# Kernel optimization log

Measured on AMD Instinct MI355X. Metric: run time of the kernel, lower is better.

The kernel has to match this reference:

```python
import jax, jax.numpy as jnp
import numpy as np

N = 8192
IN_DIM = 256
HID = 512
NUM_CLASSES = 256
AVG_DEG = 32


def setup_inputs() -> dict:
    key = jax.random.key(0)
    k_a, k_x, k_w1, k_w2 = jax.random.split(key, 4)
    # Binary adjacency with avg degree ~AVG_DEG (entries are exactly 1.0, matching
    # A.nonzero() edge extraction with implicit unit edge weights).
    A = (jax.random.uniform(k_a, (N, N)) < (AVG_DEG / N)).astype(jnp.float32)
    x = jax.random.normal(k_x, (N, IN_DIM), dtype=jnp.float32)
    # GCNConv params: glorot-ish weights, zero bias.
    W1 = jax.random.normal(k_w1, (IN_DIM, HID), dtype=jnp.float32) / np.sqrt(IN_DIM)
    b1 = jnp.zeros((HID,), dtype=jnp.float32)
    W2 = jax.random.normal(k_w2, (HID, NUM_CLASSES), dtype=jnp.float32) / np.sqrt(HID)
    b2 = jnp.zeros((NUM_CLASSES,), dtype=jnp.float32)
    sigmoid_param = jnp.array([10.0], dtype=jnp.float32)
    return {"A": A, "x": x, "W1": W1, "b1": b1, "W2": W2, "b2": b2,
            "sigmoid_param": sigmoid_param}


def _gcn_propagate(A, deg_inv_sqrt, h):
    # PyG GCNConv aggregation with self-loops, without materializing A + I:
    # out_j = d_j^{-1/2} * sum_i A_ij d_i^{-1/2} h_i  +  d_j^{-1} h_j
    m = deg_inv_sqrt[:, None] * h              # [N, d]
    agg = A.T @ m                              # messages flow row -> col
    return deg_inv_sqrt[:, None] * agg + (deg_inv_sqrt[:, None] ** 2) * h


def reference(A, x, W1, b1, W2, b2, sigmoid_param):
    # Degree from column sums of (A + I) — matches gcn_norm's scatter on col.
    deg = jnp.sum(A, axis=0) + 1.0             # [N], >= 1 thanks to self-loop
    deg_inv_sqrt = jax.lax.rsqrt(deg)
    skip_x = x                                  # nn.Identity skip connection
    # GCNConv 1: linear then normalized aggregation, then bias; ReLU.
    h = _gcn_propagate(A, deg_inv_sqrt, x @ W1) + b1
    h = jax.nn.relu(h)
    # GCNConv 2.
    h = _gcn_propagate(A, deg_inv_sqrt, h @ W2) + b2
    # Skip add + scaled sigmoid (original casts to double; kept float32 here).
    return jax.nn.sigmoid(sigmoid_param * (h + skip_x))
```

## Files before the change

kernel.cpp:

```cpp
#include <hip/hip_runtime.h>
#include <hip/hip_bf16.h>

#define N_NODES 8192
#define IN_DIM  256
#define HID     512
#define NCLS    256
#define CAP     128
#define LDSK    (HID + 8)

typedef __attribute__((ext_vector_type(8))) __bf16 bf16x8;
typedef __attribute__((ext_vector_type(4))) float  floatx4;

static __device__ __forceinline__ float bf2f(ushort u) {
    union { float f; unsigned int i; } v; v.i = ((unsigned int)u) << 16; return v.f;
}
static __device__ __forceinline__ ushort f2bf(float f) {
    __hip_bfloat16 b = __float2bfloat16(f);
    return *reinterpret_cast<ushort*>(&b);
}
static __device__ __forceinline__ void bfpair(unsigned int u, float& lo, float& hi) {
    union { float f; unsigned int i; } a, b;
    a.i = u << 16; b.i = u & 0xFFFF0000u;
    lo = a.f; hi = b.f;
}

__global__ __launch_bounds__(256) void build_csc(const float* __restrict__ A,
                                                 int* __restrict__ col_cnt,
                                                 int* __restrict__ col_idx) {
    const int jbase = (blockIdx.x * 256 + threadIdx.x) * 4;
    const int i0 = blockIdx.y * 32;
    for (int ii = 0; ii < 32; ++ii) {
        const int i = i0 + ii;
        const floatx4* p = reinterpret_cast<const floatx4*>(A + (size_t)i * N_NODES + jbase);
        floatx4 v = __builtin_nontemporal_load(p);
        if (v.x != 0.0f) { int q = atomicAdd(&col_cnt[jbase + 0], 1); if (q < CAP) col_idx[(size_t)(jbase + 0) * CAP + q] = i; }
        if (v.y != 0.0f) { int q = atomicAdd(&col_cnt[jbase + 1], 1); if (q < CAP) col_idx[(size_t)(jbase + 1) * CAP + q] = i; }
        if (v.z != 0.0f) { int q = atomicAdd(&col_cnt[jbase + 2], 1); if (q < CAP) col_idx[(size_t)(jbase + 2) * CAP + q] = i; }
        if (v.w != 0.0f) { int q = atomicAdd(&col_cnt[jbase + 3], 1); if (q < CAP) col_idx[(size_t)(jbase + 3) * CAP + q] = i; }
    }
}

__global__ __launch_bounds__(256) void prep_misc(const float* __restrict__ x,
                                                 const float* __restrict__ W1,
                                                 const float* __restrict__ W2,
                                                 const int* __restrict__ col_cnt,
                                                 ushort* __restrict__ xb,
                                                 float* __restrict__ dis,
                                                 ushort* __restrict__ W1Th, ushort* __restrict__ W1Tl,
                                                 ushort* __restrict__ W2Th, ushort* __restrict__ W2Tl) {
    const int idx = blockIdx.x * 256 + threadIdx.x;
    {
        const int i = idx * 4;
        const floatx4 v = *reinterpret_cast<const floatx4*>(x + i);
        *reinterpret_cast<ushort4*>(xb + i) = ushort4{f2bf(v.x), f2bf(v.y), f2bf(v.z), f2bf(v.w)};
    }
    if (idx < N_NODES)
        dis[idx] = rsqrtf((float)col_cnt[idx] + 1.0f);
    if (idx < IN_DIM * HID) {
        {
            const int k = idx / HID, n = idx % HID;
            const float v = W1[idx]; const ushort h = f2bf(v);
            W1Th[(size_t)n * IN_DIM + k] = h;
            W1Tl[(size_t)n * IN_DIM + k] = f2bf(v - bf2f(h));
        }
        {
            const int k = idx / NCLS, n = idx % NCLS;
            const float v = W2[idx]; const ushort h = f2bf(v);
            W2Th[(size_t)n * HID + k] = h;
            W2Tl[(size_t)n * HID + k] = f2bf(v - bf2f(h));
        }
    }
}

__global__ __launch_bounds__(256) void agg_x(const ushort* __restrict__ xb,
                                             const int* __restrict__ col_idx,
                                             const int* __restrict__ col_cnt,
                                             const float* __restrict__ dis,
                                             ushort* __restrict__ px) {
    const int j = __builtin_amdgcn_readfirstlane(blockIdx.x * 4 + (threadIdx.x >> 6));
    const int d = (threadIdx.x & 63) * 4;
    const int cnt = min(col_cnt[j], CAP);
    const float dj = dis[j];
    float a0, a1, a2, a3;
    {
        const uint2 sv = *reinterpret_cast<const uint2*>(xb + (size_t)j * IN_DIM + d);
        float f0, f1, f2, f3;
        bfpair(sv.x, f0, f1); bfpair(sv.y, f2, f3);
        a0 = dj * f0; a1 = dj * f1; a2 = dj * f2; a3 = dj * f3;
    }
    const int* __restrict__ lst = col_idx + (size_t)j * CAP;
    int e = 0;
    for (; e + 8 <= cnt; e += 8) {
        uint2 rv[8]; float we[8];
#pragma unroll
        for (int q = 0; q < 8; ++q) {
            const int i = lst[e + q];
            rv[q] = *reinterpret_cast<const uint2*>(xb + (size_t)i * IN_DIM + d);
            we[q] = dis[i];
        }
#pragma unroll
        for (int q = 0; q < 8; ++q) {
            float f0, f1, f2, f3;
            bfpair(rv[q].x, f0, f1); bfpair(rv[q].y, f2, f3);
            a0 += we[q] * f0; a1 += we[q] * f1; a2 += we[q] * f2; a3 += we[q] * f3;
        }
    }
    for (; e < cnt; ++e) {
        const int i = lst[e];
        const uint2 rv = *reinterpret_cast<const uint2*>(xb + (size_t)i * IN_DIM + d);
        const float we = dis[i];
        float f0, f1, f2, f3;
        bfpair(rv.x, f0, f1); bfpair(rv.y, f2, f3);
        a0 += we * f0; a1 += we * f1; a2 += we * f2; a3 += we * f3;
    }
    a0 *= dj; a1 *= dj; a2 *= dj; a3 *= dj;
    *reinterpret_cast<ushort4*>(px + (size_t)j * IN_DIM + d) =
        ushort4{f2bf(a0), f2bf(a1), f2bf(a2), f2bf(a3)};
}

__global__ __launch_bounds__(256) void gemm12_fused(const ushort* __restrict__ A,
                                                    const ushort* __restrict__ B1h,
                                                    const ushort* __restrict__ B1l,
                                                    const float* __restrict__ b1,
                                                    const ushort* __restrict__ B2h,
                                                    const ushort* __restrict__ B2l,
                                                    ushort* __restrict__ g2b) {
    __shared__ ushort hs[32 * LDSK];
    const int tid = threadIdx.x;
    const int lane = tid & 63, wave = tid >> 6;
    const int l16 = lane & 15, quad = lane >> 4;
    const int m_blk = blockIdx.x * 32;

    {
        const int n_base = wave * 128;
        floatx4 acc[2][8] = {};
#pragma unroll 1
        for (int k0 = 0; k0 < IN_DIM; k0 += 32) {
            const int kf = k0 + quad * 8;
            bf16x8 a[2], bh[8], bl[8];
#pragma unroll
            for (int t = 0; t < 2; ++t)
                a[t] = *reinterpret_cast<const bf16x8*>(A + (size_t)(m_blk + t * 16 + l16) * IN_DIM + kf);
#pragma unroll
            for (int t = 0; t < 8; ++t) {
                const size_t bo = (size_t)(n_base + t * 16 + l16) * IN_DIM + kf;
                bh[t] = *reinterpret_cast<const bf16x8*>(B1h + bo);
                bl[t] = *reinterpret_cast<const bf16x8*>(B1l + bo);
            }
#pragma unroll
            for (int tm = 0; tm < 2; ++tm)
#pragma unroll
                for (int tn = 0; tn < 8; ++tn) {
                    acc[tm][tn] = __builtin_amdgcn_mfma_f32_16x16x32_bf16(a[tm], bl[tn], acc[tm][tn], 0, 0, 0);
                    acc[tm][tn] = __builtin_amdgcn_mfma_f32_16x16x32_bf16(a[tm], bh[tn], acc[tm][tn], 0, 0, 0);
                }
        }
#pragma unroll
        for (int tn = 0; tn < 8; ++tn) {
            const int col = n_base + tn * 16 + l16;
            const float bv = b1[col];
#pragma unroll
            for (int tm = 0; tm < 2; ++tm)
#pragma unroll
                for (int r = 0; r < 4; ++r) {
                    const int row = tm * 16 + quad * 4 + r;
                    hs[row * LDSK + col] = f2bf(fmaxf(acc[tm][tn][r] + bv, 0.0f));
                }
        }
    }
    __syncthreads();

    {
        const int n_base = wave * 64;
        floatx4 acc[2][4] = {};
#pragma unroll 2
        for (int k0 = 0; k0 < HID; k0 += 32) {
            const int kf = k0 + quad * 8;
            bf16x8 a[2], bh[4], bl[4];
#pragma unroll
            for (int t = 0; t < 2; ++t)
                a[t] = *reinterpret_cast<const bf16x8*>(hs + (size_t)(t * 16 + l16) * LDSK + kf);
#pragma unroll
            for (int t = 0; t < 4; ++t) {
                const size_t bo = (size_t)(n_base + t * 16 + l16) * HID + kf;
                bh[t] = *reinterpret_cast<const bf16x8*>(B2h + bo);
                bl[t] = *reinterpret_cast<const bf16x8*>(B2l + bo);
            }
#pragma unroll
            for (int tm = 0; tm < 2; ++tm)
#pragma unroll
                for (int tn = 0; tn < 4; ++tn) {
                    acc[tm][tn] = __builtin_amdgcn_mfma_f32_16x16x32_bf16(a[tm], bl[tn], acc[tm][tn], 0, 0, 0);
                    acc[tm][tn] = __builtin_amdgcn_mfma_f32_16x16x32_bf16(a[tm], bh[tn], acc[tm][tn], 0, 0, 0);
                }
        }
#pragma unroll
        for (int tm = 0; tm < 2; ++tm)
#pragma unroll
            for (int tn = 0; tn < 4; ++tn)
#pragma unroll
                for (int r = 0; r < 4; ++r)
                    g2b[(size_t)(m_blk + tm * 16 + quad * 4 + r) * NCLS + (n_base + tn * 16 + l16)] =
                        f2bf(acc[tm][tn][r]);
    }
}

__global__ __launch_bounds__(256) void agg_out(const ushort* __restrict__ g2b,
                                               const int* __restrict__ col_idx,
                                               const int* __restrict__ col_cnt,
                                               const float* __restrict__ dis,
                                               const float* __restrict__ b2,
                                               const float* __restrict__ x,
                                               const float* __restrict__ sp_p,
                                               float* __restrict__ out) {
    const int j = __builtin_amdgcn_readfirstlane(blockIdx.x * 4 + (threadIdx.x >> 6));
    const int d = (threadIdx.x & 63) * 4;
    const int cnt = min(col_cnt[j], CAP);
    const float dj = dis[j];
    float a0, a1, a2, a3;
    {
        const uint2 sv = *reinterpret_cast<const uint2*>(g2b + (size_t)j * NCLS + d);
        float f0, f1, f2, f3;
        bfpair(sv.x, f0, f1); bfpair(sv.y, f2, f3);
        a0 = dj * f0; a1 = dj * f1; a2 = dj * f2; a3 = dj * f3;
    }
    const int* __restrict__ lst = col_idx + (size_t)j * CAP;
    int e = 0;
    for (; e + 8 <= cnt; e += 8) {
        uint2 rv[8]; float we[8];
#pragma unroll
        for (int q = 0; q < 8; ++q) {
            const int i = lst[e + q];
            rv[q] = *reinterpret_cast<const uint2*>(g2b + (size_t)i * NCLS + d);
            we[q] = dis[i];
        }
#pragma unroll
        for (int q = 0; q < 8; ++q) {
            float f0, f1, f2, f3;
            bfpair(rv[q].x, f0, f1); bfpair(rv[q].y, f2, f3);
            a0 += we[q] * f0; a1 += we[q] * f1; a2 += we[q] * f2; a3 += we[q] * f3;
        }
    }
    for (; e < cnt; ++e) {
        const int i = lst[e];
        const uint2 rv = *reinterpret_cast<const uint2*>(g2b + (size_t)i * NCLS + d);
        const float we = dis[i];
        float f0, f1, f2, f3;
        bfpair(rv.x, f0, f1); bfpair(rv.y, f2, f3);
        a0 += we * f0; a1 += we * f1; a2 += we * f2; a3 += we * f3;
    }
    const float sp = sp_p[0];
    const floatx4 bv = *reinterpret_cast<const floatx4*>(b2 + d);
    const floatx4 xv = __builtin_nontemporal_load(
        reinterpret_cast<const floatx4*>(x + (size_t)j * NCLS + d));
    floatx4 o;
    o.x = 1.0f / (1.0f + __expf(-sp * (dj * a0 + bv.x + xv.x)));
    o.y = 1.0f / (1.0f + __expf(-sp * (dj * a1 + bv.y + xv.y)));
    o.z = 1.0f / (1.0f + __expf(-sp * (dj * a2 + bv.z + xv.z)));
    o.w = 1.0f / (1.0f + __expf(-sp * (dj * a3 + bv.w + xv.w)));
    __builtin_nontemporal_store(o, reinterpret_cast<floatx4*>(out + (size_t)j * NCLS + d));
}

extern "C" void kernel_launch(void* const* d_in, const int* in_sizes, int n_in,
                              void* d_out, int out_size, void* d_ws, size_t ws_size,
                              hipStream_t stream) {
    const float* A  = (const float*)d_in[0];
    const float* x  = (const float*)d_in[1];
    const float* W1 = (const float*)d_in[2];
    const float* b1 = (const float*)d_in[3];
    const float* W2 = (const float*)d_in[4];
    const float* b2 = (const float*)d_in[5];
    const float* sp = (const float*)d_in[6];
    float* out = (float*)d_out;

    char* ws = (char*)d_ws;
    size_t off = 0;
    auto alloc = [&](size_t bytes) {
        void* p = ws + off;
        off = (off + bytes + 255) & ~(size_t)255;
        return p;
    };
    int*    col_cnt = (int*)   alloc((size_t)N_NODES * 4);
    float*  dis     = (float*) alloc((size_t)N_NODES * 4);
    int*    col_idx = (int*)   alloc((size_t)N_NODES * CAP * 4);
    ushort* xb      = (ushort*)alloc((size_t)N_NODES * IN_DIM * 2);
    ushort* px      = (ushort*)alloc((size_t)N_NODES * IN_DIM * 2);
    ushort* W1Th    = (ushort*)alloc((size_t)HID * IN_DIM * 2);
    ushort* W1Tl    = (ushort*)alloc((size_t)HID * IN_DIM * 2);
    ushort* W2Th    = (ushort*)alloc((size_t)NCLS * HID * 2);
    ushort* W2Tl    = (ushort*)alloc((size_t)NCLS * HID * 2);
    ushort* g2b     = (ushort*)alloc((size_t)N_NODES * NCLS * 2);

    (void)hipMemsetAsync(col_cnt, 0, (size_t)N_NODES * 4, stream);

    build_csc<<<dim3(8, 256), 256, 0, stream>>>(A, col_cnt, col_idx);
    prep_misc<<<(N_NODES * IN_DIM / 4) / 256, 256, 0, stream>>>(
        x, W1, W2, col_cnt, xb, dis, W1Th, W1Tl, W2Th, W2Tl);

    agg_x<<<N_NODES / 4, 256, 0, stream>>>(xb, col_idx, col_cnt, dis, px);
    gemm12_fused<<<N_NODES / 32, 256, 0, stream>>>(
        px, W1Th, W1Tl, b1, W2Th, W2Tl, g2b);

    agg_out<<<N_NODES / 4, 256, 0, stream>>>(g2b, col_idx, col_cnt, dis, b2, x, sp, out);
}
```

Measured before the change: 430.0 us.

## Fuse first aggregation into GEMM, merge CSC build with conversions, recompute degree norms

The standalone first-layer aggregation kernel is removed. Each GEMM block now gathers its 32 aggregated rows into shared memory before the MFMA loop, which drops the global round trip through the px buffer. The CSC build and the x/weight bf16 conversion are merged into one launch that uses extra grid rows, and the A scan now prefetches the next two rows. The dis array is gone: rsqrt of the column count is recomputed per neighbour instead. In exchange, the GEMM kernel starts with a latency-bound gather phase that runs at lower occupancy than the old separate kernel, and it needs more LDS.

```diff
diff --git a/kernel.cpp b/kernel.cpp
--- a/kernel.cpp
+++ b/kernel.cpp
@@ -6,6 +6,7 @@
 #define HID     512
 #define NCLS    256
 #define CAP     128
+#define PXK     (IN_DIM + 8)
 #define LDSK    (HID + 8)
 
 typedef __attribute__((ext_vector_type(8))) __bf16 bf16x8;
@@ -24,66 +25,16 @@
     lo = a.f; hi = b.f;
 }
 
-__global__ __launch_bounds__(256) void build_csc(const float* __restrict__ A,
-                                                 int* __restrict__ col_cnt,
-                                                 int* __restrict__ col_idx) {
-    const int jbase = (blockIdx.x * 256 + threadIdx.x) * 4;
-    const int i0 = blockIdx.y * 32;
-    for (int ii = 0; ii < 32; ++ii) {
-        const int i = i0 + ii;
-        const floatx4* p = reinterpret_cast<const floatx4*>(A + (size_t)i * N_NODES + jbase);
-        floatx4 v = __builtin_nontemporal_load(p);
-        if (v.x != 0.0f) { int q = atomicAdd(&col_cnt[jbase + 0], 1); if (q < CAP) col_idx[(size_t)(jbase + 0) * CAP + q] = i; }
-        if (v.y != 0.0f) { int q = atomicAdd(&col_cnt[jbase + 1], 1); if (q < CAP) col_idx[(size_t)(jbase + 1) * CAP + q] = i; }
-        if (v.z != 0.0f) { int q = atomicAdd(&col_cnt[jbase + 2], 1); if (q < CAP) col_idx[(size_t)(jbase + 2) * CAP + q] = i; }
-        if (v.w != 0.0f) { int q = atomicAdd(&col_cnt[jbase + 3], 1); if (q < CAP) col_idx[(size_t)(jbase + 3) * CAP + q] = i; }
-    }
-}
-
-__global__ __launch_bounds__(256) void prep_misc(const float* __restrict__ x,
-                                                 const float* __restrict__ W1,
-                                                 const float* __restrict__ W2,
-                                                 const int* __restrict__ col_cnt,
-                                                 ushort* __restrict__ xb,
-                                                 float* __restrict__ dis,
-                                                 ushort* __restrict__ W1Th, ushort* __restrict__ W1Tl,
-                                                 ushort* __restrict__ W2Th, ushort* __restrict__ W2Tl) {
-    const int idx = blockIdx.x * 256 + threadIdx.x;
-    {
-        const int i = idx * 4;
-        const floatx4 v = *reinterpret_cast<const floatx4*>(x + i);
-        *reinterpret_cast<ushort4*>(xb + i) = ushort4{f2bf(v.x), f2bf(v.y), f2bf(v.z), f2bf(v.w)};
-    }
-    if (idx < N_NODES)
-        dis[idx] = rsqrtf((float)col_cnt[idx] + 1.0f);
-    if (idx < IN_DIM * HID) {
-        {
-            const int k = idx / HID, n = idx % HID;
-            const float v = W1[idx]; const ushort h = f2bf(v);
-            W1Th[(size_t)n * IN_DIM + k] = h;
-            W1Tl[(size_t)n * IN_DIM + k] = f2bf(v - bf2f(h));
-        }
-        {
-            const int k = idx / NCLS, n = idx % NCLS;
-            const float v = W2[idx]; const ushort h = f2bf(v);
-            W2Th[(size_t)n * HID + k] = h;
-            W2Tl[(size_t)n * HID + k] = f2bf(v - bf2f(h));
-        }
-    }
-}
-
-__global__ __launch_bounds__(256) void agg_x(const ushort* __restrict__ xb,
-                                             const int* __restrict__ col_idx,
-                                             const int* __restrict__ col_cnt,
-                                             const float* __restrict__ dis,
-                                             ushort* __restrict__ px) {
-    const int j = __builtin_amdgcn_readfirstlane(blockIdx.x * 4 + (threadIdx.x >> 6));
-    const int d = (threadIdx.x & 63) * 4;
-    const int cnt = min(col_cnt[j], CAP);
-    const float dj = dis[j];
-    float a0, a1, a2, a3;
-    {
-        const uint2 sv = *reinterpret_cast<const uint2*>(xb + (size_t)j * IN_DIM + d);
+static __device__ __forceinline__ void gcn_gather256(const ushort* __restrict__ tab,
+                                                     const int* __restrict__ col_idx,
+                                                     const int* __restrict__ col_cnt,
+                                                     int j, int d,
+                                                     float& a0, float& a1, float& a2, float& a3) {
+    const int cntraw = col_cnt[j];
+    const int cnt = min(cntraw, CAP);
+    const float dj = rsqrtf((float)cntraw + 1.0f);
+    {
+        const uint2 sv = *reinterpret_cast<const uint2*>(tab + (size_t)j * 256 + d);
         float f0, f1, f2, f3;
         bfpair(sv.x, f0, f1); bfpair(sv.y, f2, f3);
         a0 = dj * f0; a1 = dj * f1; a2 = dj * f2; a3 = dj * f3;
@@ -95,8 +46,8 @@
 #pragma unroll
         for (int q = 0; q < 8; ++q) {
             const int i = lst[e + q];
-            rv[q] = *reinterpret_cast<const uint2*>(xb + (size_t)i * IN_DIM + d);
-            we[q] = dis[i];
+            rv[q] = *reinterpret_cast<const uint2*>(tab + (size_t)i * 256 + d);
+            we[q] = rsqrtf((float)col_cnt[i] + 1.0f);
         }
 #pragma unroll
         for (int q = 0; q < 8; ++q) {
@@ -107,29 +58,100 @@
     }
     for (; e < cnt; ++e) {
         const int i = lst[e];
-        const uint2 rv = *reinterpret_cast<const uint2*>(xb + (size_t)i * IN_DIM + d);
-        const float we = dis[i];
+        const uint2 rv = *reinterpret_cast<const uint2*>(tab + (size_t)i * 256 + d);
+        const float we = rsqrtf((float)col_cnt[i] + 1.0f);
         float f0, f1, f2, f3;
         bfpair(rv.x, f0, f1); bfpair(rv.y, f2, f3);
         a0 += we * f0; a1 += we * f1; a2 += we * f2; a3 += we * f3;
     }
     a0 *= dj; a1 *= dj; a2 *= dj; a3 *= dj;
-    *reinterpret_cast<ushort4*>(px + (size_t)j * IN_DIM + d) =
-        ushort4{f2bf(a0), f2bf(a1), f2bf(a2), f2bf(a3)};
-}
-
-__global__ __launch_bounds__(256) void gemm12_fused(const ushort* __restrict__ A,
+}
+
+__global__ __launch_bounds__(256) void scan_conv(const float* __restrict__ A,
+                                                 const float* __restrict__ x,
+                                                 const float* __restrict__ W1,
+                                                 const float* __restrict__ W2,
+                                                 int* __restrict__ col_cnt,
+                                                 int* __restrict__ col_idx,
+                                                 ushort* __restrict__ xb,
+                                                 ushort* __restrict__ W1Th, ushort* __restrict__ W1Tl,
+                                                 ushort* __restrict__ W2Th, ushort* __restrict__ W2Tl) {
+    if (blockIdx.y >= 256) {
+        const int idx = ((blockIdx.y - 256) * 8 + blockIdx.x) * 256 + threadIdx.x;
+        {
+            const int i = idx * 4;
+            const floatx4 v = *reinterpret_cast<const floatx4*>(x + i);
+            *reinterpret_cast<ushort4*>(xb + i) = ushort4{f2bf(v.x), f2bf(v.y), f2bf(v.z), f2bf(v.w)};
+        }
+        if (idx < IN_DIM * HID) {
+            {
+                const int k = idx / HID, n = idx % HID;
+                const float v = W1[idx]; const ushort h = f2bf(v);
+                W1Th[(size_t)n * IN_DIM + k] = h;
+                W1Tl[(size_t)n * IN_DIM + k] = f2bf(v - bf2f(h));
+            }
+            {
+                const int k = idx / NCLS, n = idx % NCLS;
+                const float v = W2[idx]; const ushort h = f2bf(v);
+                W2Th[(size_t)n * HID + k] = h;
+                W2Tl[(size_t)n * HID + k] = f2bf(v - bf2f(h));
+            }
+        }
+        return;
+    }
+    const int jbase = (blockIdx.x * 256 + threadIdx.x) * 4;
+    const int i0 = blockIdx.y * 32;
+    const float* base = A + (size_t)i0 * N_NODES + jbase;
+    floatx4 v0 = __builtin_nontemporal_load(reinterpret_cast<const floatx4*>(base));
+    floatx4 v1 = __builtin_nontemporal_load(reinterpret_cast<const floatx4*>(base + N_NODES));
+#define PROC(v, irow) do { \
+    if ((v).x != 0.0f) { int q = atomicAdd(&col_cnt[jbase + 0], 1); if (q < CAP) col_idx[(size_t)(jbase + 0) * CAP + q] = (irow); } \
+    if ((v).y != 0.0f) { int q = atomicAdd(&col_cnt[jbase + 1], 1); if (q < CAP) col_idx[(size_t)(jbase + 1) * CAP + q] = (irow); } \
+    if ((v).z != 0.0f) { int q = atomicAdd(&col_cnt[jbase + 2], 1); if (q < CAP) col_idx[(size_t)(jbase + 2) * CAP + q] = (irow); } \
+    if ((v).w != 0.0f) { int q = atomicAdd(&col_cnt[jbase + 3], 1); if (q < CAP) col_idx[(size_t)(jbase + 3) * CAP + q] = (irow); } \
+} while (0)
+    for (int ii = 0; ii < 32; ii += 2) {
+        floatx4 n0 = {}, n1 = {};
+        if (ii + 2 < 32) {
+            n0 = __builtin_nontemporal_load(reinterpret_cast<const floatx4*>(base + (size_t)(ii + 2) * N_NODES));
+            n1 = __builtin_nontemporal_load(reinterpret_cast<const floatx4*>(base + (size_t)(ii + 3) * N_NODES));
+        }
+        PROC(v0, i0 + ii);
+        PROC(v1, i0 + ii + 1);
+        v0 = n0; v1 = n1;
+    }
+#undef PROC
+}
+
+__global__ __launch_bounds__(256) void gemm12_fused(const ushort* __restrict__ xb,
+                                                    const int* __restrict__ col_idx,
+                                                    const int* __restrict__ col_cnt,
                                                     const ushort* __restrict__ B1h,
                                                     const ushort* __restrict__ B1l,
                                                     const float* __restrict__ b1,
                                                     const ushort* __restrict__ B2h,
                                                     const ushort* __restrict__ B2l,
                                                     ushort* __restrict__ g2b) {
-    __shared__ ushort hs[32 * LDSK];
+    __shared__ __align__(16) ushort pxs[32 * PXK];
+    __shared__ __align__(16) ushort hs[32 * LDSK];
     const int tid = threadIdx.x;
     const int lane = tid & 63, wave = tid >> 6;
     const int l16 = lane & 15, quad = lane >> 4;
     const int m_blk = blockIdx.x * 32;
+
+    {
+        const int d = lane * 4;
+#pragma unroll 1
+        for (int s = 0; s < 8; ++s) {
+            const int jl = wave * 8 + s;
+            const int j = __builtin_amdgcn_readfirstlane(m_blk + jl);
+            float a0, a1, a2, a3;
+            gcn_gather256(xb, col_idx, col_cnt, j, d, a0, a1, a2, a3);
+            *reinterpret_cast<ushort4*>(&pxs[jl * PXK + d]) =
+                ushort4{f2bf(a0), f2bf(a1), f2bf(a2), f2bf(a3)};
+        }
+    }
+    __syncthreads();
 
     {
         const int n_base = wave * 128;
@@ -140,7 +162,7 @@
             bf16x8 a[2], bh[8], bl[8];
 #pragma unroll
             for (int t = 0; t < 2; ++t)
-                a[t] = *reinterpret_cast<const bf16x8*>(A + (size_t)(m_blk + t * 16 + l16) * IN_DIM + kf);
+                a[t] = *reinterpret_cast<const bf16x8*>(pxs + (size_t)(t * 16 + l16) * PXK + kf);
 #pragma unroll
             for (int t = 0; t < 8; ++t) {
                 const size_t bo = (size_t)(n_base + t * 16 + l16) * IN_DIM + kf;
@@ -208,56 +230,23 @@
 __global__ __launch_bounds__(256) void agg_out(const ushort* __restrict__ g2b,
                                                const int* __restrict__ col_idx,
                                                const int* __restrict__ col_cnt,
-                                               const float* __restrict__ dis,
                                                const float* __restrict__ b2,
                                                const float* __restrict__ x,
                                                const float* __restrict__ sp_p,
                                                float* __restrict__ out) {
     const int j = __builtin_amdgcn_readfirstlane(blockIdx.x * 4 + (threadIdx.x >> 6));
     const int d = (threadIdx.x & 63) * 4;
-    const int cnt = min(col_cnt[j], CAP);
-    const float dj = dis[j];
     float a0, a1, a2, a3;
-    {
-        const uint2 sv = *reinterpret_cast<const uint2*>(g2b + (size_t)j * NCLS + d);
-        float f0, f1, f2, f3;
-        bfpair(sv.x, f0, f1); bfpair(sv.y, f2, f3);
-        a0 = dj * f0; a1 = dj * f1; a2 = dj * f2; a3 = dj * f3;
-    }
-    const int* __restrict__ lst = col_idx + (size_t)j * CAP;
-    int e = 0;
-    for (; e + 8 <= cnt; e += 8) {
-        uint2 rv[8]; float we[8];
-#pragma unroll
-        for (int q = 0; q < 8; ++q) {
-            const int i = lst[e + q];
-            rv[q] = *reinterpret_cast<const uint2*>(g2b + (size_t)i * NCLS + d);
-            we[q] = dis[i];
-        }
-#pragma unroll
-        for (int q = 0; q < 8; ++q) {
-            float f0, f1, f2, f3;
-            bfpair(rv[q].x, f0, f1); bfpair(rv[q].y, f2, f3);
-            a0 += we[q] * f0; a1 += we[q] * f1; a2 += we[q] * f2; a3 += we[q] * f3;
-        }
-    }
-    for (; e < cnt; ++e) {
-        const int i = lst[e];
-        const uint2 rv = *reinterpret_cast<const uint2*>(g2b + (size_t)i * NCLS + d);
-        const float we = dis[i];
-        float f0, f1, f2, f3;
-        bfpair(rv.x, f0, f1); bfpair(rv.y, f2, f3);
-        a0 += we * f0; a1 += we * f1; a2 += we * f2; a3 += we * f3;
-    }
+    gcn_gather256(g2b, col_idx, col_cnt, j, d, a0, a1, a2, a3);
     const float sp = sp_p[0];
     const floatx4 bv = *reinterpret_cast<const floatx4*>(b2 + d);
     const floatx4 xv = __builtin_nontemporal_load(
         reinterpret_cast<const floatx4*>(x + (size_t)j * NCLS + d));
     floatx4 o;
-    o.x = 1.0f / (1.0f + __expf(-sp * (dj * a0 + bv.x + xv.x)));
-    o.y = 1.0f / (1.0f + __expf(-sp * (dj * a1 + bv.y + xv.y)));
-    o.z = 1.0f / (1.0f + __expf(-sp * (dj * a2 + bv.z + xv.z)));
-    o.w = 1.0f / (1.0f + __expf(-sp * (dj * a3 + bv.w + xv.w)));
+    o.x = 1.0f / (1.0f + __expf(-sp * (a0 + bv.x + xv.x)));
+    o.y = 1.0f / (1.0f + __expf(-sp * (a1 + bv.y + xv.y)));
+    o.z = 1.0f / (1.0f + __expf(-sp * (a2 + bv.z + xv.z)));
+    o.w = 1.0f / (1.0f + __expf(-sp * (a3 + bv.w + xv.w)));
     __builtin_nontemporal_store(o, reinterpret_cast<floatx4*>(out + (size_t)j * NCLS + d));
 }
 
@@ -281,10 +270,8 @@
         return p;
     };
     int*    col_cnt = (int*)   alloc((size_t)N_NODES * 4);
-    float*  dis     = (float*) alloc((size_t)N_NODES * 4);
     int*    col_idx = (int*)   alloc((size_t)N_NODES * CAP * 4);
     ushort* xb      = (ushort*)alloc((size_t)N_NODES * IN_DIM * 2);
-    ushort* px      = (ushort*)alloc((size_t)N_NODES * IN_DIM * 2);
     ushort* W1Th    = (ushort*)alloc((size_t)HID * IN_DIM * 2);
     ushort* W1Tl    = (ushort*)alloc((size_t)HID * IN_DIM * 2);
     ushort* W2Th    = (ushort*)alloc((size_t)NCLS * HID * 2);
@@ -293,13 +280,11 @@
 
     (void)hipMemsetAsync(col_cnt, 0, (size_t)N_NODES * 4, stream);
 
-    build_csc<<<dim3(8, 256), 256, 0, stream>>>(A, col_cnt, col_idx);
-    prep_misc<<<(N_NODES * IN_DIM / 4) / 256, 256, 0, stream>>>(
-        x, W1, W2, col_cnt, xb, dis, W1Th, W1Tl, W2Th, W2Tl);
-
-    agg_x<<<N_NODES / 4, 256, 0, stream>>>(xb, col_idx, col_cnt, dis, px);
+    scan_conv<<<dim3(8, 512), 256, 0, stream>>>(
+        A, x, W1, W2, col_cnt, col_idx, xb, W1Th, W1Tl, W2Th, W2Tl);
+
     gemm12_fused<<<N_NODES / 32, 256, 0, stream>>>(
-        px, W1Th, W1Tl, b1, W2Th, W2Tl, g2b);
-
-    agg_out<<<N_NODES / 4, 256, 0, stream>>>(g2b, col_idx, col_cnt, dis, b2, x, sp, out);
-}
+        xb, col_idx, col_cnt, W1Th, W1Tl, b1, W2Th, W2Tl, g2b);
+
+    agg_out<<<N_NODES / 4, 256, 0, stream>>>(g2b, col_idx, col_cnt, b2, x, sp, out);
+}
```

After: 444.1 us. 1.03x slower.
